# Optimization experiments

Measured on AMD Instinct MI355X. Metric: run time of the kernel, lower is better.

Reference implementation:

```python
import jax, jax.numpy as jnp
import numpy as np

B, H, W = 2, 240, 320
C_ENC, C_SEG = 64, 21
TRUNC = 3
REP = 2 * TRUNC + 1
DMIN, DMAX = 0.4, 6.0
VOXEL = 0.03
FDIMS = 256.0
FX = FY = 300.0


def _point_sample(feat, grid):
    # feat: [C, Hf, Wf]; grid: [N, 2] = (x, y) in [0, 1].
    # Matches F.grid_sample(feat, 2*grid-1, bilinear, zeros, align_corners=False).
    Cc, Hf, Wf = feat.shape
    ix = grid[:, 0] * Wf - 0.5
    iy = grid[:, 1] * Hf - 0.5
    x0 = jnp.floor(ix)
    y0 = jnp.floor(iy)
    wx = ix - x0
    wy = iy - y0

    def gather(xi, yi):
        valid = (xi >= 0) & (xi < Wf) & (yi >= 0) & (yi < Hf)
        xc = jnp.clip(xi, 0, Wf - 1).astype(jnp.int32)
        yc = jnp.clip(yi, 0, Hf - 1).astype(jnp.int32)
        return feat[:, yc, xc] * valid.astype(feat.dtype)

    return (gather(x0, y0) * ((1 - wx) * (1 - wy))
            + gather(x0 + 1, y0) * (wx * (1 - wy))
            + gather(x0, y0 + 1) * ((1 - wx) * wy)
            + gather(x0 + 1, y0 + 1) * (wx * wy))  # [C, N]


def _single(depth, enc, seg, intr):
    f32 = depth.dtype
    K_inv = jnp.linalg.inv(intr)

    # generate_frustum: image corners unprojected at depth_min / depth_max.
    cpx = jnp.array([[0., 0.], [W, 0.], [0., H], [W, H]], f32)

    def unproj(z):
        p = jnp.concatenate([cpx * z, jnp.full((4, 1), z, f32), jnp.ones((4, 1), f32)], -1)
        return (K_inv @ p.T).T[:, :3]

    corners = jnp.concatenate([unproj(DMIN), unproj(DMAX)], 0)  # [8, 3]
    fmin = corners.min(0)
    fmax = corners.max(0)
    # compute_camera2frustum_transform: scale to voxels, shift frustum min to origin.
    c2f = (jnp.eye(4, dtype=f32)
           .at[jnp.arange(3), jnp.arange(3)].set(1.0 / VOXEL)
           .at[:3, 3].set(-fmin / VOXEL))
    pad_off = (FDIMS - (fmax - fmin) / VOXEL) * 0.5  # [3]

    # depth clipping (dense mask instead of nonzero; invalid rows zeroed at end)
    valid = (depth >= DMIN) & (depth <= DMAX)
    z = jnp.where(valid, depth, 0.0).reshape(-1)  # [N]
    yy, xx = jnp.meshgrid(jnp.arange(H, dtype=f32), jnp.arange(W, dtype=f32), indexing='ij')
    xy = jnp.stack([xx.reshape(-1), yy.reshape(-1)], -1)  # [N, 2] (x, y)
    norm_xy = xy / jnp.array([W, H], f32)
    xv_yv = norm_xy * jnp.array([W, H], f32) * z[:, None]  # image_size = (W, H)
    feat_grid = xy / jnp.array([W, H], f32)  # feat_size covers full image

    pix = jnp.concatenate([xv_yv, z[:, None], jnp.ones_like(z)[:, None]], -1).T  # [4, N]
    gc = (c2f @ (K_inv @ pix)).T[:, :3]  # [N, 3] frustum-grid coords
    cz = gc[:, 2]
    offs = jnp.arange(-TRUNC, TRUNC + 1, dtype=f32)  # [REP]
    coords = gc[:, None, :] + offs[None, :, None] * jnp.array([0., 0., 1.], f32)
    flat_coords = coords.reshape(-1, 3) + pad_off  # [N*REP, 3]

    # truncated df values: frac(z) + offset, then sign/abs channels
    df = (cz - jnp.trunc(cz))[:, None] + offs[None, :]  # [N, REP]
    df = jnp.stack([jnp.sign(df), jnp.abs(df)], -1)  # [N, REP, 2]

    seg_f = _point_sample(seg, norm_xy).T   # [N, C_SEG]
    enc_f = _point_sample(enc, feat_grid).T  # [N, C_ENC]
    samp = jnp.concatenate([enc_f, seg_f], -1)  # [N, C_ENC+C_SEG]
    samp = jnp.broadcast_to(samp[:, None, :], (H * W, REP, C_ENC + C_SEG))
    feats = jnp.concatenate([df, samp], -1).reshape(-1, 2 + C_ENC + C_SEG)  # [N*REP, D]

    m = jnp.broadcast_to(valid.reshape(-1)[:, None], (H * W, REP)).reshape(-1, 1).astype(f32)
    return jnp.concatenate([feats * m, flat_coords * m], -1)  # [N*REP, D+3]


def setup_inputs() -> dict:
    key = jax.random.key(0)
    k1, k2, k3 = jax.random.split(key, 3)
    depth = jax.random.uniform(k1, (B, H, W), minval=0.2, maxval=6.2)
    enc = jax.random.normal(k2, (B, C_ENC, H // 2, W // 2), dtype=jnp.float32)
    seg = jax.random.normal(k3, (B, C_SEG, H, W), dtype=jnp.float32)
    K = np.eye(4, dtype=np.float32)
    K[0, 0] = FX; K[1, 1] = FY; K[0, 2] = W / 2.0; K[1, 2] = H / 2.0
    intrinsic = jnp.asarray(np.broadcast_to(K, (B, 4, 4)).copy())
    return {"depth": depth, "encoder_features": enc, "sem_seg": seg, "intrinsic": intrinsic}


def reference(depth, encoder_features, sem_seg, intrinsic):
    # [B, H*W*REP, 2 + C_ENC + C_SEG + 3] = sparse features ++ frustum coordinates
    return jax.vmap(_single)(depth, encoder_features, sem_seg, intrinsic)
```

## Files before the change

kernel.cpp:

```cpp
#include <hip/hip_runtime.h>
#include <math.h>

#define BPIX 64
#define HW   76800
#define W_   320
#define H_   240
#define ENC_W 160
#define ENC_H 120
#define CENC 64
#define CSEG 21
#define NCH  85
#define ROW  90
#define PIXF 630
#define PIXF2 315

__global__ void setup_consts_kernel(const float* __restrict__ intr,
                                    float* __restrict__ C) {
  int b = threadIdx.x;
  if (b >= 2) return;
  float A[4][4], inv[4][4];
  for (int r = 0; r < 4; ++r)
    for (int c = 0; c < 4; ++c) {
      A[r][c] = intr[b * 16 + r * 4 + c];
      inv[r][c] = (r == c) ? 1.f : 0.f;
    }
  for (int k = 0; k < 4; ++k) {
    int piv = k; float best = fabsf(A[k][k]);
    for (int r = k + 1; r < 4; ++r) {
      float v = fabsf(A[r][k]);
      if (v > best) { best = v; piv = r; }
    }
    if (piv != k) {
      for (int c = 0; c < 4; ++c) {
        float t = A[k][c]; A[k][c] = A[piv][c]; A[piv][c] = t;
        t = inv[k][c]; inv[k][c] = inv[piv][c]; inv[piv][c] = t;
      }
    }
    float ip = 1.f / A[k][k];
    for (int c = 0; c < 4; ++c) { A[k][c] *= ip; inv[k][c] *= ip; }
    for (int r = 0; r < 4; ++r) if (r != k) {
      float f = A[r][k];
      for (int c = 0; c < 4; ++c) { A[r][c] -= f * A[k][c]; inv[r][c] -= f * inv[k][c]; }
    }
  }
  const float cpx[4][2] = {{0.f, 0.f}, {320.f, 0.f}, {0.f, 240.f}, {320.f, 240.f}};
  float fmn[3] = {1e30f, 1e30f, 1e30f}, fmx[3] = {-1e30f, -1e30f, -1e30f};
  for (int zi = 0; zi < 2; ++zi) {
    float z = zi ? 6.0f : 0.4f;
    for (int i = 0; i < 4; ++i) {
      float px = cpx[i][0] * z, py = cpx[i][1] * z;
      for (int ax = 0; ax < 3; ++ax) {
        float v = inv[ax][0] * px + inv[ax][1] * py + inv[ax][2] * z + inv[ax][3];
        fmn[ax] = fminf(fmn[ax], v);
        fmx[ax] = fmaxf(fmx[ax], v);
      }
    }
  }
  float* Cb = C + b * 32;
  for (int r = 0; r < 4; ++r)
    for (int c = 0; c < 4; ++c) Cb[r * 4 + c] = inv[r][c];
  for (int ax = 0; ax < 3; ++ax) {
    Cb[16 + ax] = -fmn[ax] / 0.03f;
    Cb[19 + ax] = (256.0f - (fmx[ax] - fmn[ax]) / 0.03f) * 0.5f;
  }
}

__global__ __launch_bounds__(256) void sparse_proj_kernel(
    const float* __restrict__ depth, const float* __restrict__ enc,
    const float* __restrict__ seg, const float* __restrict__ C,
    float* __restrict__ out) {
  __shared__ float sampM[BPIX * NCH];
  __shared__ float mArr[BPIX], fracArr[BPIX], fc0[BPIX], fc1[BPIX], fc2[BPIX];
  __shared__ int   eo0[BPIX], eo1[BPIX], eo2[BPIX], eo3[BPIX];
  __shared__ float ew0[BPIX], ew1[BPIX], ew2[BPIX], ew3[BPIX];
  __shared__ int   so0[BPIX], so1[BPIX], so2[BPIX], so3[BPIX];
  __shared__ float sw0[BPIX], sw1[BPIX], sw2[BPIX], sw3[BPIX];

  const int tid = threadIdx.x;
  const int bx = blockIdx.x;
  const int b  = blockIdx.y;
  const float* Cb = C + b * 32;

  if (tid < BPIX) {
    const int p = tid;
    const int gpix = bx * BPIX + p;
    const int x = gpix % W_;
    const int y = gpix / W_;
    const float d = depth[(size_t)b * HW + gpix];
    const bool val = (d >= 0.4f) && (d <= 6.0f);
    const float m = val ? 1.f : 0.f;
    const float z = val ? d : 0.f;
    const float nx = (float)x / 320.f;
    const float ny = (float)y / 240.f;
    const float xv = nx * 320.f * z;
    const float yv = ny * 240.f * z;
    const float q0 = Cb[0] * xv + Cb[1] * yv + Cb[2] * z + Cb[3];
    const float q1 = Cb[4] * xv + Cb[5] * yv + Cb[6] * z + Cb[7];
    const float q2 = Cb[8] * xv + Cb[9] * yv + Cb[10] * z + Cb[11];
    const float q3 = Cb[12] * xv + Cb[13] * yv + Cb[14] * z + Cb[15];
    const float INV_V = (float)(1.0 / 0.03);
    const float gcx = q0 * INV_V + Cb[16] * q3;
    const float gcy = q1 * INV_V + Cb[17] * q3;
    const float gcz = q2 * INV_V + Cb[18] * q3;
    mArr[p] = m;
    fracArr[p] = gcz - truncf(gcz);
    fc0[p] = (gcx + Cb[19]) * m;
    fc1[p] = (gcy + Cb[20]) * m;
    fc2[p] = (gcz + Cb[21]) * m;
    {
      const float ix = nx * 160.f - 0.5f;
      const float iy = ny * 120.f - 0.5f;
      const float x0f = floorf(ix), y0f = floorf(iy);
      const float wx = ix - x0f, wy = iy - y0f;
      const int x0 = (int)x0f, y0 = (int)y0f;
      const int x1 = x0 + 1, y1 = y0 + 1;
      const float vx0 = (x0 >= 0 && x0 < 160) ? 1.f : 0.f;
      const float vx1 = (x1 >= 0 && x1 < 160) ? 1.f : 0.f;
      const float vy0 = (y0 >= 0 && y0 < 120) ? 1.f : 0.f;
      const float vy1 = (y1 >= 0 && y1 < 120) ? 1.f : 0.f;
      const int xc0 = min(max(x0, 0), 159), xc1 = min(max(x1, 0), 159);
      const int yc0 = min(max(y0, 0), 119), yc1 = min(max(y1, 0), 119);
      eo0[p] = yc0 * 160 + xc0; ew0[p] = (1.f - wx) * (1.f - wy) * vx0 * vy0;
      eo1[p] = yc0 * 160 + xc1; ew1[p] = wx * (1.f - wy) * vx1 * vy0;
      eo2[p] = yc1 * 160 + xc0; ew2[p] = (1.f - wx) * wy * vx0 * vy1;
      eo3[p] = yc1 * 160 + xc1; ew3[p] = wx * wy * vx1 * vy1;
    }
    {
      const float ix = nx * 320.f - 0.5f;
      const float iy = ny * 240.f - 0.5f;
      const float x0f = floorf(ix), y0f = floorf(iy);
      const float wx = ix - x0f, wy = iy - y0f;
      const int x0 = (int)x0f, y0 = (int)y0f;
      const int x1 = x0 + 1, y1 = y0 + 1;
      const float vx0 = (x0 >= 0 && x0 < 320) ? 1.f : 0.f;
      const float vx1 = (x1 >= 0 && x1 < 320) ? 1.f : 0.f;
      const float vy0 = (y0 >= 0 && y0 < 240) ? 1.f : 0.f;
      const float vy1 = (y1 >= 0 && y1 < 240) ? 1.f : 0.f;
      const int xc0 = min(max(x0, 0), 319), xc1 = min(max(x1, 0), 319);
      const int yc0 = min(max(y0, 0), 239), yc1 = min(max(y1, 0), 239);
      so0[p] = yc0 * 320 + xc0; sw0[p] = (1.f - wx) * (1.f - wy) * vx0 * vy0;
      so1[p] = yc0 * 320 + xc1; sw1[p] = wx * (1.f - wy) * vx1 * vy0;
      so2[p] = yc1 * 320 + xc0; sw2[p] = (1.f - wx) * wy * vx0 * vy1;
      so3[p] = yc1 * 320 + xc1; sw3[p] = wx * wy * vx1 * vy1;
    }
  }
  __syncthreads();

  for (int idx = tid; idx < BPIX * NCH; idx += 256) {
    const int p = idx & (BPIX - 1);
    const int ch = idx >> 6;
    float v;
    if (ch < CENC) {
      const float* fb = enc + ((size_t)b * CENC + ch) * (ENC_H * ENC_W);
      v = ew0[p] * fb[eo0[p]] + ew1[p] * fb[eo1[p]] +
          ew2[p] * fb[eo2[p]] + ew3[p] * fb[eo3[p]];
    } else {
      const float* fb = seg + ((size_t)b * CSEG + (ch - CENC)) * (size_t)HW;
      v = sw0[p] * fb[so0[p]] + sw1[p] * fb[so1[p]] +
          sw2[p] * fb[so2[p]] + sw3[p] * fb[so3[p]];
    }
    sampM[p * NCH + ch] = v * mArr[p];
  }
  __syncthreads();

  float2* out2 = reinterpret_cast<float2*>(out + (size_t)(b * HW + bx * BPIX) * PIXF);
  for (int j = tid; j < BPIX * PIXF2; j += 256) {
    const int p = j / PIXF2;
    const int t2 = j - p * PIXF2;
    const int fi = t2 * 2;
    const int r = fi / ROW;
    const int c = fi - r * ROW;
    const float m = mArr[p];
    float2 v;
    if (c == 0) {
      const float df = fracArr[p] + (float)(r - 3);
      const float s = (df > 0.f) ? 1.f : ((df < 0.f) ? -1.f : 0.f);
      v.x = s * m;
      v.y = fabsf(df) * m;
    } else if (c < 86) {
      v.x = sampM[p * NCH + (c - 2)];
      v.y = sampM[p * NCH + (c - 1)];
    } else if (c == 86) {
      v.x = sampM[p * NCH + 84];
      v.y = fc0[p];
    } else {
      v.x = fc1[p];
      v.y = fc2[p] + (float)(r - 3) * m;
    }
    out2[j] = v;
  }
}

extern "C" void kernel_launch(void* const* d_in, const int* in_sizes, int n_in,
                              void* d_out, int out_size, void* d_ws, size_t ws_size,
                              hipStream_t stream) {
  const float* depth = (const float*)d_in[0];
  const float* enc   = (const float*)d_in[1];
  const float* seg   = (const float*)d_in[2];
  const float* intr  = (const float*)d_in[3];
  float* out = (float*)d_out;
  float* C   = (float*)d_ws;

  setup_consts_kernel<<<1, 64, 0, stream>>>(intr, C);
  dim3 grid(HW / BPIX, 2);
  sparse_proj_kernel<<<grid, 256, 0, stream>>>(depth, enc, seg, C, out);
}
```

Measured before the change: 454.7 us.

## Vectorize output writes with float4 nontemporal stores and per-pixel LDS template

Restructures the final write loop to emit 16-byte nontemporal stores instead of float2 stores. A per-pixel template row is built in shared memory, and per-repeat sign/abs and z coordinates are precomputed so that most vectors are a direct copy. Index math switches to magic-multiply division, and the three setup tasks are spread across three thread groups instead of one. The cost is more shared memory and a slower per-element path for vectors that straddle row boundaries.

```diff
diff --git a/kernel.cpp b/kernel.cpp
--- a/kernel.cpp
+++ b/kernel.cpp
@@ -12,7 +12,10 @@
 #define NCH  85
 #define ROW  90
 #define PIXF 630
-#define PIXF2 315
+#define TPLS 94
+#define NF4  10080
+
+typedef float f4v __attribute__((ext_vector_type(4)));
 
 __global__ void setup_consts_kernel(const float* __restrict__ intr,
                                     float* __restrict__ C) {
@@ -69,29 +72,32 @@
     const float* __restrict__ depth, const float* __restrict__ enc,
     const float* __restrict__ seg, const float* __restrict__ C,
     float* __restrict__ out) {
-  __shared__ float sampM[BPIX * NCH];
-  __shared__ float mArr[BPIX], fracArr[BPIX], fc0[BPIX], fc1[BPIX], fc2[BPIX];
-  __shared__ int   eo0[BPIX], eo1[BPIX], eo2[BPIX], eo3[BPIX];
-  __shared__ float ew0[BPIX], ew1[BPIX], ew2[BPIX], ew3[BPIX];
-  __shared__ int   so0[BPIX], so1[BPIX], so2[BPIX], so3[BPIX];
-  __shared__ float sw0[BPIX], sw1[BPIX], sw2[BPIX], sw3[BPIX];
+  __shared__ float  tpl[BPIX * TPLS];
+  __shared__ float2 sd[BPIX * 7];
+  __shared__ float  fcz[BPIX * 7];
+  __shared__ float  mArr[BPIX];
+  __shared__ int    eo0[BPIX], eo1[BPIX], eo2[BPIX], eo3[BPIX];
+  __shared__ float  ew0[BPIX], ew1[BPIX], ew2[BPIX], ew3[BPIX];
+  __shared__ int    so0[BPIX], so1[BPIX], so2[BPIX], so3[BPIX];
+  __shared__ float  sw0[BPIX], sw1[BPIX], sw2[BPIX], sw3[BPIX];
 
   const int tid = threadIdx.x;
-  const int bx = blockIdx.x;
-  const int b  = blockIdx.y;
+  const int bx  = blockIdx.x;
+  const int b   = blockIdx.y;
   const float* Cb = C + b * 32;
-
-  if (tid < BPIX) {
-    const int p = tid;
-    const int gpix = bx * BPIX + p;
-    const int x = gpix % W_;
-    const int y = gpix / W_;
-    const float d = depth[(size_t)b * HW + gpix];
+  const int x0 = (bx % 5) * 64;
+  const int yrow = bx / 5;
+
+  const int grp = tid >> 6;
+  const int p   = tid & 63;
+
+  if (grp == 0) {
+    const float d = depth[(size_t)b * HW + bx * BPIX + p];
     const bool val = (d >= 0.4f) && (d <= 6.0f);
     const float m = val ? 1.f : 0.f;
     const float z = val ? d : 0.f;
-    const float nx = (float)x / 320.f;
-    const float ny = (float)y / 240.f;
+    const float nx = (float)(x0 + p) / 320.f;
+    const float ny = (float)yrow / 240.f;
     const float xv = nx * 320.f * z;
     const float yv = ny * 240.f * z;
     const float q0 = Cb[0] * xv + Cb[1] * yv + Cb[2] * z + Cb[3];
@@ -103,91 +109,105 @@
     const float gcy = q1 * INV_V + Cb[17] * q3;
     const float gcz = q2 * INV_V + Cb[18] * q3;
     mArr[p] = m;
-    fracArr[p] = gcz - truncf(gcz);
-    fc0[p] = (gcx + Cb[19]) * m;
-    fc1[p] = (gcy + Cb[20]) * m;
-    fc2[p] = (gcz + Cb[21]) * m;
-    {
-      const float ix = nx * 160.f - 0.5f;
-      const float iy = ny * 120.f - 0.5f;
-      const float x0f = floorf(ix), y0f = floorf(iy);
-      const float wx = ix - x0f, wy = iy - y0f;
-      const int x0 = (int)x0f, y0 = (int)y0f;
-      const int x1 = x0 + 1, y1 = y0 + 1;
-      const float vx0 = (x0 >= 0 && x0 < 160) ? 1.f : 0.f;
-      const float vx1 = (x1 >= 0 && x1 < 160) ? 1.f : 0.f;
-      const float vy0 = (y0 >= 0 && y0 < 120) ? 1.f : 0.f;
-      const float vy1 = (y1 >= 0 && y1 < 120) ? 1.f : 0.f;
-      const int xc0 = min(max(x0, 0), 159), xc1 = min(max(x1, 0), 159);
-      const int yc0 = min(max(y0, 0), 119), yc1 = min(max(y1, 0), 119);
-      eo0[p] = yc0 * 160 + xc0; ew0[p] = (1.f - wx) * (1.f - wy) * vx0 * vy0;
-      eo1[p] = yc0 * 160 + xc1; ew1[p] = wx * (1.f - wy) * vx1 * vy0;
-      eo2[p] = yc1 * 160 + xc0; ew2[p] = (1.f - wx) * wy * vx0 * vy1;
-      eo3[p] = yc1 * 160 + xc1; ew3[p] = wx * wy * vx1 * vy1;
-    }
-    {
-      const float ix = nx * 320.f - 0.5f;
-      const float iy = ny * 240.f - 0.5f;
-      const float x0f = floorf(ix), y0f = floorf(iy);
-      const float wx = ix - x0f, wy = iy - y0f;
-      const int x0 = (int)x0f, y0 = (int)y0f;
-      const int x1 = x0 + 1, y1 = y0 + 1;
-      const float vx0 = (x0 >= 0 && x0 < 320) ? 1.f : 0.f;
-      const float vx1 = (x1 >= 0 && x1 < 320) ? 1.f : 0.f;
-      const float vy0 = (y0 >= 0 && y0 < 240) ? 1.f : 0.f;
-      const float vy1 = (y1 >= 0 && y1 < 240) ? 1.f : 0.f;
-      const int xc0 = min(max(x0, 0), 319), xc1 = min(max(x1, 0), 319);
-      const int yc0 = min(max(y0, 0), 239), yc1 = min(max(y1, 0), 239);
-      so0[p] = yc0 * 320 + xc0; sw0[p] = (1.f - wx) * (1.f - wy) * vx0 * vy0;
-      so1[p] = yc0 * 320 + xc1; sw1[p] = wx * (1.f - wy) * vx1 * vy0;
-      so2[p] = yc1 * 320 + xc0; sw2[p] = (1.f - wx) * wy * vx0 * vy1;
-      so3[p] = yc1 * 320 + xc1; sw3[p] = wx * wy * vx1 * vy1;
-    }
+    tpl[p * TPLS + 87] = (gcx + Cb[19]) * m;
+    tpl[p * TPLS + 88] = (gcy + Cb[20]) * m;
+    const float fr = gcz - truncf(gcz);
+    const float fz = (gcz + Cb[21]) * m;
+#pragma unroll
+    for (int r = 0; r < 7; ++r) {
+      const float df = fr + (float)(r - 3);
+      const float s = (df > 0.f) ? 1.f : ((df < 0.f) ? -1.f : 0.f);
+      sd[p * 7 + r] = make_float2(s * m, fabsf(df) * m);
+      fcz[p * 7 + r] = fz + (float)(r - 3) * m;
+    }
+  } else if (grp == 1) {
+    const float nx = (float)(x0 + p) / 320.f;
+    const float ny = (float)yrow / 240.f;
+    const float ix = nx * 160.f - 0.5f;
+    const float iy = ny * 120.f - 0.5f;
+    const float x0f = floorf(ix), y0f = floorf(iy);
+    const float wx = ix - x0f, wy = iy - y0f;
+    const int xi0 = (int)x0f, yi0 = (int)y0f;
+    const int xi1 = xi0 + 1, yi1 = yi0 + 1;
+    const float vx0 = (xi0 >= 0 && xi0 < ENC_W) ? 1.f : 0.f;
+    const float vx1 = (xi1 >= 0 && xi1 < ENC_W) ? 1.f : 0.f;
+    const float vy0 = (yi0 >= 0 && yi0 < ENC_H) ? 1.f : 0.f;
+    const float vy1 = (yi1 >= 0 && yi1 < ENC_H) ? 1.f : 0.f;
+    const int xc0 = min(max(xi0, 0), ENC_W - 1), xc1 = min(max(xi1, 0), ENC_W - 1);
+    const int yc0 = min(max(yi0, 0), ENC_H - 1), yc1 = min(max(yi1, 0), ENC_H - 1);
+    eo0[p] = yc0 * ENC_W + xc0; ew0[p] = (1.f - wx) * (1.f - wy) * vx0 * vy0;
+    eo1[p] = yc0 * ENC_W + xc1; ew1[p] = wx * (1.f - wy) * vx1 * vy0;
+    eo2[p] = yc1 * ENC_W + xc0; ew2[p] = (1.f - wx) * wy * vx0 * vy1;
+    eo3[p] = yc1 * ENC_W + xc1; ew3[p] = wx * wy * vx1 * vy1;
+  } else if (grp == 2) {
+    const float nx = (float)(x0 + p) / 320.f;
+    const float ny = (float)yrow / 240.f;
+    const float ix = nx * 320.f - 0.5f;
+    const float iy = ny * 240.f - 0.5f;
+    const float x0f = floorf(ix), y0f = floorf(iy);
+    const float wx = ix - x0f, wy = iy - y0f;
+    const int xi0 = (int)x0f, yi0 = (int)y0f;
+    const int xi1 = xi0 + 1, yi1 = yi0 + 1;
+    const float vx0 = (xi0 >= 0 && xi0 < W_) ? 1.f : 0.f;
+    const float vx1 = (xi1 >= 0 && xi1 < W_) ? 1.f : 0.f;
+    const float vy0 = (yi0 >= 0 && yi0 < H_) ? 1.f : 0.f;
+    const float vy1 = (yi1 >= 0 && yi1 < H_) ? 1.f : 0.f;
+    const int xc0 = min(max(xi0, 0), W_ - 1), xc1 = min(max(xi1, 0), W_ - 1);
+    const int yc0 = min(max(yi0, 0), H_ - 1), yc1 = min(max(yi1, 0), H_ - 1);
+    so0[p] = yc0 * W_ + xc0; sw0[p] = (1.f - wx) * (1.f - wy) * vx0 * vy0;
+    so1[p] = yc0 * W_ + xc1; sw1[p] = wx * (1.f - wy) * vx1 * vy0;
+    so2[p] = yc1 * W_ + xc0; sw2[p] = (1.f - wx) * wy * vx0 * vy1;
+    so3[p] = yc1 * W_ + xc1; sw3[p] = wx * wy * vx1 * vy1;
   }
   __syncthreads();
 
   for (int idx = tid; idx < BPIX * NCH; idx += 256) {
-    const int p = idx & (BPIX - 1);
+    const int pp = idx & (BPIX - 1);
     const int ch = idx >> 6;
     float v;
     if (ch < CENC) {
       const float* fb = enc + ((size_t)b * CENC + ch) * (ENC_H * ENC_W);
-      v = ew0[p] * fb[eo0[p]] + ew1[p] * fb[eo1[p]] +
-          ew2[p] * fb[eo2[p]] + ew3[p] * fb[eo3[p]];
+      v = ew0[pp] * fb[eo0[pp]] + ew1[pp] * fb[eo1[pp]] +
+          ew2[pp] * fb[eo2[pp]] + ew3[pp] * fb[eo3[pp]];
     } else {
       const float* fb = seg + ((size_t)b * CSEG + (ch - CENC)) * (size_t)HW;
-      v = sw0[p] * fb[so0[p]] + sw1[p] * fb[so1[p]] +
-          sw2[p] * fb[so2[p]] + sw3[p] * fb[so3[p]];
-    }
-    sampM[p * NCH + ch] = v * mArr[p];
+      v = sw0[pp] * fb[so0[pp]] + sw1[pp] * fb[so1[pp]] +
+          sw2[pp] * fb[so2[pp]] + sw3[pp] * fb[so3[pp]];
+    }
+    tpl[pp * TPLS + 2 + ch] = v * mArr[pp];
   }
   __syncthreads();
 
-  float2* out2 = reinterpret_cast<float2*>(out + (size_t)(b * HW + bx * BPIX) * PIXF);
-  for (int j = tid; j < BPIX * PIXF2; j += 256) {
-    const int p = j / PIXF2;
-    const int t2 = j - p * PIXF2;
-    const int fi = t2 * 2;
-    const int r = fi / ROW;
-    const int c = fi - r * ROW;
-    const float m = mArr[p];
-    float2 v;
-    if (c == 0) {
-      const float df = fracArr[p] + (float)(r - 3);
-      const float s = (df > 0.f) ? 1.f : ((df < 0.f) ? -1.f : 0.f);
-      v.x = s * m;
-      v.y = fabsf(df) * m;
-    } else if (c < 86) {
-      v.x = sampM[p * NCH + (c - 2)];
-      v.y = sampM[p * NCH + (c - 1)];
-    } else if (c == 86) {
-      v.x = sampM[p * NCH + 84];
-      v.y = fc0[p];
+  f4v* out4 = reinterpret_cast<f4v*>(out + (size_t)(b * HW + bx * BPIX) * PIXF);
+  for (int j = tid; j < NF4; j += 256) {
+    const unsigned e0 = (unsigned)j << 2;
+    const int pq = (int)((e0 * 53262u) >> 25);
+    const int w  = (int)e0 - pq * 630;
+    const int r  = (int)(((unsigned)w * 729u) >> 16);
+    const int c  = w - r * 90;
+    f4v v;
+    if ((unsigned)(c - 2) <= 83u) {
+      const float2* t = reinterpret_cast<const float2*>(&tpl[pq * TPLS + c]);
+      const float2 a = t[0];
+      const float2 bq = t[1];
+      v.x = a.x; v.y = a.y; v.z = bq.x; v.w = bq.y;
     } else {
-      v.x = fc1[p];
-      v.y = fc2[p] + (float)(r - 3) * m;
-    }
-    out2[j] = v;
+#pragma unroll
+      for (int k = 0; k < 4; ++k) {
+        const unsigned e = e0 + (unsigned)k;
+        const int pk = (int)((e * 53262u) >> 25);
+        const int wk = (int)e - pk * 630;
+        const int rk = (int)(((unsigned)wk * 729u) >> 16);
+        const int ck = wk - rk * 90;
+        float val;
+        if (ck == 0)       val = sd[pk * 7 + rk].x;
+        else if (ck == 1)  val = sd[pk * 7 + rk].y;
+        else if (ck == 89) val = fcz[pk * 7 + rk];
+        else               val = tpl[pk * TPLS + ck];
+        v[k] = val;
+      }
+    }
+    __builtin_nontemporal_store(v, &out4[j]);
   }
 }
 
```

New measurement: 463.3 us. Within noise of the previous version (+1.9%).
